# Kernel optimization log

Hardware: AMD Instinct MI355X
Metric: run time of the kernel (lower is better)

## Reference

```python
import jax, jax.numpy as jnp
import numpy as np

# ---- static physical configuration (matches init_kwargs param dict) ----
NX = NY = 513
NL = 3
N_ENS = 4
LX = LY = 5120.0e3
DX = LX / (NX - 1)
DY = LY / (NY - 1)
F0 = 9.375e-5
BETA = 1.754e-11
A2 = 0.0
A4 = 2.0e9
DELTA_EK = 2.0
TAU0 = 2.0e-5
BCCO = 0.2
ZFBC = BCCO / (1.0 + 0.5 * BCCO)
DT = 600.0
NUM_STEPS = 4
HEIGHTS = np.array([350.0, 750.0, 2900.0])
RED_G = np.array([0.025, 0.0125])

JAC_COEF = 1.0 / (F0 * DX * DY)
HYPERDIFF_COEF = A4 / F0**2 / DX**6
BOTTOM_FRICTION_COEF = DELTA_EK / (2.0 * abs(F0) * DX**2 * (-HEIGHTS[-1]))


def _build_constants():
    """Precompute stratification / mode / Helmholtz matrices (float64 numpy, cast to f32)."""
    A = np.zeros((NL, NL))
    A[0, 0] = 1.0 / (HEIGHTS[0] * RED_G[0])
    A[0, 1] = -1.0 / (HEIGHTS[0] * RED_G[0])
    for i in range(1, NL - 1):
        A[i, i - 1] = -1.0 / (HEIGHTS[i] * RED_G[i - 1])
        A[i, i] = 1.0 / HEIGHTS[i] * (1.0 / RED_G[i] + 1.0 / RED_G[i - 1])
        A[i, i + 1] = -1.0 / (HEIGHTS[i] * RED_G[i])
    A[-1, -1] = 1.0 / (HEIGHTS[NL - 1] * RED_G[NL - 2])
    A[-1, -2] = -1.0 / (HEIGHTS[NL - 1] * RED_G[NL - 2])
    lam_r, R = np.linalg.eig(A)
    lam_l, L = np.linalg.eig(A.T)
    lam_r, R, lam_l, L = lam_r.real, R.real, lam_l.real, L.real
    # align left eigenvectors with right eigenvalue ordering (biorthogonality)
    order = np.array([int(np.argmin(np.abs(lam_l - lr))) for lr in lam_r])
    L = L[:, order]
    Cl2m = np.diag(1.0 / np.diag(L.T @ R)) @ L.T
    Cm2l = R
    lambd = lam_r
    # DST-I eigenvalues of the 5-point Laplacian on the interior grid
    xg, yg = np.meshgrid(np.arange(1, NX - 1), np.arange(1, NY - 1), indexing='ij')
    lap_dst = (2 * (np.cos(np.pi / (NX - 1) * xg) - 1) / DX**2
               + 2 * (np.cos(np.pi / (NY - 1) * yg) - 1) / DY**2)
    helm_dst = lap_dst[None] / F0**2 - lambd[:, None, None]  # (nl, nx-2, ny-2)

    def np_dstI1D(x):
        N = x.shape[-1]
        xp = np.zeros(x.shape[:-1] + (N + 2,))
        xp[..., 1:-1] = x
        return np.fft.irfft(-1j * xp, n=2 * (N + 1), axis=-1, norm='ortho')[..., 1:N + 1]

    def np_dstI2D(x):
        return np.swapaxes(np_dstI1D(np.swapaxes(np_dstI1D(x), -1, -2)), -1, -2)

    const = np.ones((NL, NX, NY)) / (NX * NY)
    s = np.zeros_like(const)
    s[:, 1:-1, 1:-1] = np_dstI2D(np_dstI2D(const[:, 1:-1, 1:-1]) / helm_dst)
    hom_sol = (const + s * lambd[:, None, None])[:-1]  # (nl-1, nx, ny)
    M = (Cm2l[1:] - Cm2l[:-1])[:NL - 1, :NL - 1] * hom_sol.mean((1, 2))[None, :]
    alpha = -np.linalg.inv(M) @ (Cm2l[1:, :-1] - Cm2l[:-1, :-1])
    # wind forcing: curl(tau)/(f0*H1) on interior points; tau_y = 0, tau_x(y) only
    tau_x = -TAU0 * np.cos(2 * np.pi * (np.arange(NY) + 0.5) / NY)[None, :] * np.ones((NX, NY))
    dtaux_dy = (tau_x[1:-1, 2:] - tau_x[1:-1, :-2]) / (2 * DY)
    wind = (-dtaux_dy / (F0 * HEIGHTS[0]))[None]  # (1, nx-2, ny-2)
    f32 = lambda a: jnp.asarray(a, jnp.float32)
    return dict(A=f32(A), Cl2m=f32(Cl2m), Cm2l=f32(Cm2l), helmoltz_dst=f32(helm_dst),
                alpha_matrix=f32(alpha), homogeneous_sol=f32(hom_sol), wind_forcing=f32(wind))


# ---------------- stencil ops ----------------

def _pad11(x):
    return jnp.pad(x, [(0, 0)] * (x.ndim - 2) + [(1, 1), (1, 1)])


def laplacian_h_nobc(f):
    # unscaled 5-point Laplacian, interior values only: (..., nx-2, ny-2)
    return (f[..., 2:, 1:-1] + f[..., :-2, 1:-1] + f[..., 1:-1, 2:] + f[..., 1:-1, :-2]
            - 4.0 * f[..., 1:-1, 1:-1])


def laplacian_h(f, fc):
    # full-grid Laplacian with partial-slip boundary treatment (coefficient fc = zfbc)
    lap = _pad11(laplacian_h_nobc(f))
    lap = lap.at[..., 0, :].set(fc * (f[..., 1, :] - f[..., 0, :]))
    lap = lap.at[..., -1, :].set(fc * (f[..., -2, :] - f[..., -1, :]))
    lap = lap.at[..., :, 0].set(fc * (f[..., :, 1] - f[..., :, 0]))
    lap = lap.at[..., :, -1].set(fc * (f[..., :, -2] - f[..., :, -1]))
    return lap


def laplacian_h_boundaries(f, fc):
    # boundary Laplacian values, concat order: x=0 (y interior), x=-1, y=0 (full x), y=-1
    return jnp.concatenate([
        fc * (f[..., 1, 1:-1] - f[..., 0, 1:-1]),
        fc * (f[..., -2, 1:-1] - f[..., -1, 1:-1]),
        fc * (f[..., :, 1] - f[..., :, 0]),
        fc * (f[..., :, -2] - f[..., :, -1])], axis=-1)


def jacobi_h(f, g):
    # Arakawa 9-point Jacobian J(f, g), interior values (..., nx-2, ny-2)
    dx_f = f[..., 2:, :] - f[..., :-2, :]
    dx_g = g[..., 2:, :] - g[..., :-2, :]
    dy_f = f[..., 2:] - f[..., :-2]
    dy_g = g[..., 2:] - g[..., :-2]
    return ((dx_f[..., 1:-1] * dy_g[..., 1:-1, :] - dx_g[..., 1:-1] * dy_f[..., 1:-1, :])
            + (f[..., 2:, 1:-1] * dy_g[..., 2:, :] - f[..., :-2, 1:-1] * dy_g[..., :-2, :])
            - (f[..., 1:-1, 2:] * dx_g[..., 2:] - f[..., 1:-1, :-2] * dx_g[..., :-2])
            + (g[..., 1:-1, 2:] * dx_f[..., 2:] - g[..., 1:-1, :-2] * dx_f[..., :-2])
            - (g[..., 2:, 1:-1] * dy_f[..., 2:, :] - g[..., :-2, 1:-1] * dy_f[..., :-2, :])) / 12.0


# ---------------- DST-I elliptic solve ----------------

def dstI1D(x):
    N = x.shape[-1]
    z = jnp.zeros(x.shape[:-1] + (1,), x.dtype)
    xp = jnp.concatenate([z, x, z], axis=-1)
    return jnp.fft.irfft(-1j * xp.astype(jnp.complex64), n=2 * (N + 1), axis=-1,
                         norm='ortho')[..., 1:N + 1]


def dstI2D(x):
    return jnp.swapaxes(dstI1D(jnp.swapaxes(dstI1D(x), -1, -2)), -1, -2)


def inverse_elliptic_dst(f, op_dst):
    return dstI2D(dstI2D(f) / op_dst)


# ---------------- QG time derivative ----------------

def _time_derivatives(y, A, Cl2m, Cm2l, helm_dst, alpha, hom_sol, wind):
    q, p = y[0], y[1]  # (..., nl, nx, ny)
    # advection + hyperdiffusion RHS on interior (a_2 == 0 branch skipped as in source)
    rhs = JAC_COEF * jacobi_h(q, p)
    delta2_p = laplacian_h(p, ZFBC)
    rhs = rhs - HYPERDIFF_COEF * laplacian_h_nobc(laplacian_h(delta2_p, ZFBC))
    rhs = rhs.at[..., 0:1, :, :].add(wind)
    rhs = rhs.at[..., -1:, :, :].add(BOTTOM_FRICTION_COEF * laplacian_h_nobc(p[..., -1:, :, :]))
    dq = _pad11(rhs)
    # layers -> modes, DST Helmholtz inversion, homogeneous-solution correction
    rhs_h = jnp.einsum('ij,...jxy->...ixy', Cl2m, dq)
    dp_modes = _pad11(inverse_elliptic_dst(rhs_h[..., 1:-1, 1:-1], helm_dst))
    mean_m = dp_modes[..., :-1, :, :].mean((-2, -1))  # (..., nl-1)
    dalpha = jnp.einsum('ij,...j->...i', alpha, mean_m)[..., None, None]
    dp_modes = dp_modes.at[..., :-1, :, :].add(dalpha * hom_sol)
    dp = jnp.einsum('ij,...jxy->...ixy', Cm2l, dp_modes)
    # boundary vorticity update
    dp_bound = jnp.concatenate([dp[..., 0, 1:-1], dp[..., -1, 1:-1],
                                dp[..., :, 0], dp[..., :, -1]], axis=-1)
    delta_p_bound = laplacian_h_boundaries(dp / (F0 * DX)**2, ZFBC)
    dq_bound = delta_p_bound - jnp.einsum('ij,...jl->...il', A, dp_bound)
    ny2 = NY - 2
    dq = dq.at[..., 0, 1:-1].set(dq_bound[..., :ny2])
    dq = dq.at[..., -1, 1:-1].set(dq_bound[..., ny2:2 * ny2])
    dq = dq.at[..., :, 0].set(dq_bound[..., 2 * ny2:2 * ny2 + NX])
    dq = dq.at[..., :, -1].set(dq_bound[..., 2 * ny2 + NX:2 * ny2 + 2 * NX])
    return jnp.stack((dq, dp), 0)


def _forecast(y0, t, A, Cl2m, Cm2l, helm_dst, alpha, hom_sol, wind):
    deriv = lambda y: _time_derivatives(y, A, Cl2m, Cm2l, helm_dst, alpha, hom_sol, wind)

    def step(y, dt_):
        k1 = deriv(y)
        k2 = deriv(y + 0.5 * dt_ * k1)
        k3 = deriv(y + 0.5 * dt_ * k2)
        k4 = deriv(y + dt_ * k3)
        y_next = y + (dt_ / 6.0) * (k1 + 2.0 * k2 + 2.0 * k3 + k4)
        return y_next, y_next

    _, traj = jax.lax.scan(step, y0, t[1:] - t[:-1])
    return jnp.concatenate([y0[None], traj], axis=0)  # (T, 2, n_ens, nl, nx, ny)


def setup_inputs() -> dict:
    key = jax.random.key(0)
    y0 = 0.1 * jax.random.normal(key, (2, N_ENS, NL, NX, NY), dtype=jnp.float32)
    t = jnp.arange(NUM_STEPS + 1, dtype=jnp.float32) * DT
    consts = _build_constants()
    return dict(y0=y0, t=t, **consts)


def reference(y0, t, A, Cl2m, Cm2l, helmoltz_dst, alpha_matrix, homogeneous_sol, wind_forcing):
    return _forecast(y0, t, A, Cl2m, Cm2l, helmoltz_dst, alpha_matrix,
                     homogeneous_sol, wind_forcing)
```

## Files before the change

### kernel.cpp

```cpp
#include <hip/hip_runtime.h>
#include <math.h>

#define NXY 513
#define NIN 511
#define NL3 3
#define NE4 4
#define NB 12
#define GLD 512

static constexpr long FS  = (long)NE4 * NL3 * NXY * NXY;
static constexpr long GSZ = (long)NB * GLD * GLD;
static constexpr int  NSTEPS = 4;

static constexpr double dF0 = 9.375e-05;
static constexpr double dDX = 10000.0;
static constexpr float ZFBCf     = (float)(0.2 / (1.0 + 0.5 * 0.2));
static constexpr float JACCf     = (float)(1.0 / (dF0 * dDX * dDX));
static constexpr float HYPCf     = (float)(2.0e9 / (dF0 * dF0) / (dDX*dDX*dDX*dDX*dDX*dDX));
static constexpr float BFCf      = (float)(2.0 / (2.0 * dF0 * dDX * dDX * (-2900.0)));
static constexpr float INVF0DX2f = (float)(1.0 / ((dF0 * dDX) * (dF0 * dDX)));

typedef short  bf16x8 __attribute__((ext_vector_type(8)));
typedef float  f32x4  __attribute__((ext_vector_type(4)));
typedef unsigned int u32;
typedef __attribute__((address_space(1))) const u32 GAS;
typedef __attribute__((address_space(3))) u32 LAS;
#define GLDS(gp, lp) __builtin_amdgcn_global_load_lds((GAS*)(gp), (LAS*)(lp), 16, 0, 0)

__device__ __forceinline__ unsigned short f2bf(float x) {
    unsigned int u = __float_as_uint(x);
    return (unsigned short)((u + 0x7FFFu + ((u >> 16) & 1u)) >> 16);
}
__device__ __forceinline__ float bf2f(unsigned short h) {
    return __uint_as_float(((unsigned int)h) << 16);
}

__global__ void initS_kernel(unsigned short* __restrict__ Sh, unsigned short* __restrict__ Sl) {
    int k = blockIdx.x * 256 + threadIdx.x;
    int n = blockIdx.y;
    if (k >= GLD || n >= GLD) return;
    float v = 0.f;
    if (n < NIN && k < NIN) {
        int m = ((n + 1) * (k + 1)) & 1023;
        v = (float)(0.0625 * sin(M_PI * (double)m / 512.0));
    }
    unsigned short hs = f2bf(v);
    Sh[n * GLD + k] = hs;
    Sl[n * GLD + k] = f2bf(v - bf2f(hs));
}

__global__ __launch_bounds__(256) void fused_rhs(
    float* __restrict__ kq, const float* __restrict__ q, const float* __restrict__ p,
    const float* __restrict__ wind)
{
    __shared__ float ps[22][72];
    __shared__ float qs[22][72];
    __shared__ float l1[22][72];
    __shared__ float l2[22][72];
    const int c  = blockIdx.z;
    const int x0 = 1 + blockIdx.y * 16;
    const int y0 = 1 + blockIdx.x * 64;
    const int t  = threadIdx.x;
    const size_t off = (size_t)c * NXY * NXY;
    const float* pp = p + off;
    const float* qp = q + off;

    for (int idx = t; idx < 22 * 70; idx += 256) {
        int i = idx / 70, j = idx % 70;
        int gx = x0 - 3 + i, gy = y0 - 3 + j;
        bool in = (gx >= 0 && gx < NXY && gy >= 0 && gy < NXY);
        size_t go = (size_t)gx * NXY + gy;
        ps[i][j] = in ? pp[go] : 0.f;
        qs[i][j] = in ? qp[go] : 0.f;
    }
    __syncthreads();

#define LAPBC(a, i, j, gx, gy) \
    ((gy) == 0       ? ZFBCf * (a[i][(j)+1] - a[i][j]) : \
     (gy) == NXY-1   ? ZFBCf * (a[i][(j)-1] - a[i][j]) : \
     (gx) == 0       ? ZFBCf * (a[(i)+1][j] - a[i][j]) : \
     (gx) == NXY-1   ? ZFBCf * (a[(i)-1][j] - a[i][j]) : \
     a[(i)+1][j] + a[(i)-1][j] + a[i][(j)+1] + a[i][(j)-1] - 4.f * a[i][j])

    for (int idx = t; idx < 20 * 68; idx += 256) {
        int i = 1 + idx / 68, j = 1 + idx % 68;
        int gx = x0 - 3 + i, gy = y0 - 3 + j;
        float v = 0.f;
        if (gx >= 0 && gx < NXY && gy >= 0 && gy < NXY) v = LAPBC(ps, i, j, gx, gy);
        l1[i][j] = v;
    }
    __syncthreads();

    for (int idx = t; idx < 18 * 66; idx += 256) {
        int i = 2 + idx / 66, j = 2 + idx % 66;
        int gx = x0 - 3 + i, gy = y0 - 3 + j;
        float v = 0.f;
        if (gx >= 0 && gx < NXY && gy >= 0 && gy < NXY) v = LAPBC(l1, i, j, gx, gy);
        l2[i][j] = v;
    }
    __syncthreads();
#undef LAPBC

    const int l = c % NL3;
    for (int idx = t; idx < 16 * 64; idx += 256) {
        int i = 3 + idx / 64, j = 3 + idx % 64;
        int gx = x0 - 3 + i, gy = y0 - 3 + j;
        if (gx > NIN || gy > NIN) continue;
        float fmm=qs[i-1][j-1], fm0=qs[i-1][j], fmp=qs[i-1][j+1];
        float f0m=qs[i][j-1],                    f0p=qs[i][j+1];
        float fpm=qs[i+1][j-1], fp0=qs[i+1][j], fpp=qs[i+1][j+1];
        float gmm=ps[i-1][j-1], gm0=ps[i-1][j], gmp=ps[i-1][j+1];
        float g0m=ps[i][j-1],   g00=ps[i][j],   g0p=ps[i][j+1];
        float gpm=ps[i+1][j-1], gp0=ps[i+1][j], gpp=ps[i+1][j+1];
        float J1 = (fp0 - fm0) * (g0p - g0m) - (gp0 - gm0) * (f0p - f0m);
        float J2 = fp0 * (gpp - gpm) - fm0 * (gmp - gmm);
        float J3 = f0p * (gpp - gmp) - f0m * (gpm - gmm);
        float J4 = g0p * (fpp - fmp) - g0m * (fpm - fmm);
        float J5 = gp0 * (fpp - fpm) - gm0 * (fmp - fmm);
        float jac = (J1 + J2 - J3 + J4 - J5) * (1.0f / 12.0f);
        float lap3 = l2[i+1][j] + l2[i-1][j] + l2[i][j+1] + l2[i][j-1] - 4.f * l2[i][j];
        float v = JACCf * jac - HYPCf * lap3;
        if (l == 0)       v += wind[(size_t)(gx-1) * NIN + (gy-1)];
        if (l == NL3-1)   v += BFCf * (gp0 + gm0 + g0p + g0m - 4.f * g00);
        kq[off + (size_t)gx * NXY + gy] = v;
    }
}

__global__ void l2m_kernel(unsigned short* __restrict__ Gh, unsigned short* __restrict__ Gl,
                           const float* __restrict__ kq, const float* __restrict__ Cl2m) {
    int ry = blockIdx.x * blockDim.x + threadIdx.x;
    int rx = blockIdx.y * blockDim.y + threadIdx.y;
    int e = blockIdx.z;
    size_t go = (size_t)(e * NL3) * GLD * GLD + (size_t)rx * GLD + ry;
    if (rx >= NIN || ry >= NIN) {
        for (int i = 0; i < 3; ++i) { Gh[go + (size_t)i*GLD*GLD] = 0; Gl[go + (size_t)i*GLD*GLD] = 0; }
        return;
    }
    size_t base = ((size_t)(e * NL3) * NXY + (rx + 1)) * NXY + (ry + 1);
    float f0 = kq[base];
    float f1 = kq[base + (size_t)NXY*NXY];
    float f2 = kq[base + 2*(size_t)NXY*NXY];
    float v[3];
    v[0] = Cl2m[0]*f0 + Cl2m[1]*f1 + Cl2m[2]*f2;
    v[1] = Cl2m[3]*f0 + Cl2m[4]*f1 + Cl2m[5]*f2;
    v[2] = Cl2m[6]*f0 + Cl2m[7]*f1 + Cl2m[8]*f2;
#pragma unroll
    for (int i = 0; i < 3; ++i) {
        unsigned short hs = f2bf(v[i]);
        Gh[go + (size_t)i*GLD*GLD] = hs;
        Gl[go + (size_t)i*GLD*GLD] = f2bf(v[i] - bf2f(hs));
    }
}

#define EPLD 68
__global__ __launch_bounds__(256, 3) void gemm_dst(
    const unsigned short* __restrict__ Ah, const unsigned short* __restrict__ Al,
    const unsigned short* __restrict__ Sh, const unsigned short* __restrict__ Sl,
    unsigned short* __restrict__ Ch, unsigned short* __restrict__ Cl,
    float* __restrict__ Cf, const float* __restrict__ helm)
{
    __shared__ __attribute__((aligned(16))) char ldsraw[32768];
    float* ep = (float*)ldsraw;
    const int id = blockIdx.x;
    const int nblk = id / 96, rr = id - nblk * 96;
    const int b = rr >> 3, mblk = rr & 7;
    const int m0 = mblk << 6, n0 = nblk << 6;
    const int t = threadIdx.x;
    const int wave = t >> 6, lane = t & 63;
    const int wr = wave >> 1, wc = wave & 1;
    const int lr = lane & 15, g = lane >> 4;
    const unsigned short* Abh = Ah + (size_t)b * 262144;
    const unsigned short* Abl = Al + (size_t)b * 262144;

    const int srow = t >> 2;
    const int scol = ((t & 3) ^ ((srow >> 1) & 3)) * 8;
    const size_t gAe = (size_t)(m0 + srow) * 512 + scol;
    const size_t gBe = (size_t)(n0 + srow) * 512 + scol;
    const int ldbase = wave * 1024;

    auto STAGE = [&](int buf, int kt) {
        char* bb = ldsraw + buf * 16384;
        int ke = kt * 32;
        GLDS(Abh + gAe + ke, bb + ldbase);
        GLDS(Abl + gAe + ke, bb + 4096 + ldbase);
        GLDS(Sh  + gBe + ke, bb + 8192 + ldbase);
        GLDS(Sl  + gBe + ke, bb + 12288 + ldbase);
    };

    f32x4 acc[2][2] = {};
    int abyte[2], bbyte[2];
#pragma unroll
    for (int i = 0; i < 2; ++i) {
        int ar = wr*32 + i*16 + lr;
        abyte[i] = ar*64 + ((g ^ ((ar >> 1) & 3)) * 16);
    }
#pragma unroll
    for (int j = 0; j < 2; ++j) {
        int br = wc*32 + j*16 + lr;
        bbyte[j] = 8192 + br*64 + ((g ^ ((br >> 1) & 3)) * 16);
    }

    STAGE(0, 0);
    __syncthreads();
    for (int it = 0; it < 16; ++it) {
        const int buf = it & 1;
        if (it < 15) STAGE(buf ^ 1, it + 1);
        const char* bb = ldsraw + buf * 16384;
        bf16x8 fbh[2], fbl[2];
#pragma unroll
        for (int j = 0; j < 2; ++j) {
            fbh[j] = *(const bf16x8*)(bb + bbyte[j]);
            fbl[j] = *(const bf16x8*)(bb + 4096 + bbyte[j]);
        }
#pragma unroll
        for (int i = 0; i < 2; ++i) {
            bf16x8 fah = *(const bf16x8*)(bb + abyte[i]);
            bf16x8 fal = *(const bf16x8*)(bb + 4096 + abyte[i]);
#pragma unroll
            for (int j = 0; j < 2; ++j) {
                acc[i][j] = __builtin_amdgcn_mfma_f32_16x16x32_bf16(fah, fbh[j], acc[i][j], 0, 0, 0);
                acc[i][j] = __builtin_amdgcn_mfma_f32_16x16x32_bf16(fah, fbl[j], acc[i][j], 0, 0, 0);
                acc[i][j] = __builtin_amdgcn_mfma_f32_16x16x32_bf16(fal, fbh[j], acc[i][j], 0, 0, 0);
            }
        }
        __syncthreads();
    }

    const int mode = b % NL3;
    const float* hp = helm ? (helm + (size_t)mode * NIN * NIN) : nullptr;
#pragma unroll
    for (int i = 0; i < 2; ++i) {
        int mml = wr*32 + i*16 + 4*g;
#pragma unroll
        for (int j = 0; j < 2; ++j) {
            int nnl = wc*32 + j*16 + lr;
            int nn = n0 + nnl;
            float v[4];
#pragma unroll
            for (int r = 0; r < 4; ++r) v[r] = acc[i][j][r];
            if (hp && nn < NIN) {
                int mmb = m0 + mml;
#pragma unroll
                for (int r = 0; r < 4; ++r)
                    if (mmb + r < NIN) v[r] /= hp[(size_t)nn*NIN + mmb + r];
            }
#pragma unroll
            for (int r = 0; r < 4; ++r) ep[nnl*EPLD + mml + r] = v[r];
        }
    }
    __syncthreads();

#pragma unroll
    for (int c = 0; c < 2; ++c) {
        int chunk = t + 256*c;
        int row = chunk >> 3;
        int cb  = (chunk & 7) * 8;
        float v[8];
#pragma unroll
        for (int k = 0; k < 8; ++k) v[k] = ep[row*EPLD + cb + k];
        size_t co = (size_t)b*262144 + (size_t)(n0 + row)*512 + m0 + cb;
        if (Cf) {
            f32x4 v0 = {v[0], v[1], v[2], v[3]};
            f32x4 v1 = {v[4], v[5], v[6], v[7]};
            *(f32x4*)(Cf + co)     = v0;
            *(f32x4*)(Cf + co + 4) = v1;
        } else {
            unsigned int h[4], lo[4];
#pragma unroll
            for (int k = 0; k < 4; ++k) {
                unsigned short h0 = f2bf(v[2*k]), h1 = f2bf(v[2*k+1]);
                unsigned short l0 = f2bf(v[2*k]-bf2f(h0)), l1 = f2bf(v[2*k+1]-bf2f(h1));
                h[k]  = (unsigned int)h0 | ((unsigned int)h1 << 16);
                lo[k] = (unsigned int)l0 | ((unsigned int)l1 << 16);
            }
            *(uint4*)(Ch + co) = make_uint4(h[0], h[1], h[2], h[3]);
            *(uint4*)(Cl + co) = make_uint4(lo[0], lo[1], lo[2], lo[3]);
        }
    }
}

__global__ void mean_kernel(float* __restrict__ partial, const float* __restrict__ G) {
    int gy = blockIdx.y;
    int e = gy >> 1, m = gy & 1;
    const float* g = G + (size_t)(e * NL3 + m) * GLD * GLD;
    float s = 0.f;
    for (int idx = blockIdx.x * 256 + threadIdx.x; idx < GLD*GLD; idx += 64 * 256)
        s += g[idx];
    __shared__ float red[256];
    red[threadIdx.x] = s; __syncthreads();
    for (int w = 128; w >= 1; w >>= 1) {
        if (threadIdx.x < w) red[threadIdx.x] += red[threadIdx.x + w];
        __syncthreads();
    }
    if (threadIdx.x == 0) partial[gy * 64 + blockIdx.x] = red[0];
}

__global__ void dalpha_kernel(float* __restrict__ dal, const float* __restrict__ partial,
                              const float* __restrict__ alpha) {
    int t = threadIdx.x;
    if (t >= 8) return;
    int e = t >> 1, i = t & 1;
    float s0 = 0.f, s1 = 0.f;
    for (int bk = 0; bk < 64; ++bk) { s0 += partial[(e*2+0)*64 + bk]; s1 += partial[(e*2+1)*64 + bk]; }
    const float inv = 1.0f / ((float)NXY * (float)NXY);
    dal[t] = alpha[i*2+0] * (s0 * inv) + alpha[i*2+1] * (s1 * inv);
}

__global__ void m2l_kernel(float* __restrict__ kp, const float* __restrict__ G,
                           const float* __restrict__ dal, const float* __restrict__ hom,
                           const float* __restrict__ Cm2l) {
    int y = blockIdx.x * blockDim.x + threadIdx.x;
    int x = blockIdx.y * blockDim.y + threadIdx.y;
    int e = blockIdx.z;
    if (x >= NXY || y >= NXY) return;
    float mv[3];
    bool interior = (x >= 1 && x <= NIN && y >= 1 && y <= NIN);
#pragma unroll
    for (int i = 0; i < 3; ++i)
        mv[i] = interior ? G[(size_t)(e*NL3 + i) * GLD * GLD + (size_t)(x-1) * GLD + (y-1)] : 0.f;
    float h0 = hom[(size_t)x * NXY + y];
    float h1 = hom[(size_t)NXY*NXY + (size_t)x * NXY + y];
    mv[0] += dal[e*2 + 0] * h0;
    mv[1] += dal[e*2 + 1] * h1;
#pragma unroll
    for (int l = 0; l < 3; ++l)
        kp[((size_t)(e*NL3 + l) * NXY + x) * NXY + y] =
            Cm2l[l*3+0]*mv[0] + Cm2l[l*3+1]*mv[1] + Cm2l[l*3+2]*mv[2];
}

__global__ void bound_kernel(float* __restrict__ kq, const float* __restrict__ kp,
                             const float* __restrict__ Amat) {
    int pos = blockIdx.x * 256 + threadIdx.x;
    int e = blockIdx.y;
    if (pos >= 2048) return;
    int x, y, xn, yn;
    if (pos < NIN)            { x = 0;      y = pos + 1;        xn = 1;      yn = y; }
    else if (pos < 2*NIN)     { x = NXY-1;  y = pos - NIN + 1;  xn = NXY-2;  yn = y; }
    else if (pos < 2*NIN+NXY) { x = pos - 2*NIN;       y = 0;      xn = x; yn = 1; }
    else                      { x = pos - (2*NIN+NXY); y = NXY-1;  xn = x; yn = NXY-2; }
    float dpb[3], lpb[3];
#pragma unroll
    for (int j = 0; j < 3; ++j) {
        const float* f = kp + (size_t)(e*NL3 + j) * NXY * NXY;
        float c = f[(size_t)x * NXY + y];
        float nb = f[(size_t)xn * NXY + yn];
        dpb[j] = c;
        lpb[j] = ZFBCf * INVF0DX2f * (nb - c);
    }
#pragma unroll
    for (int l = 0; l < 3; ++l) {
        float v = lpb[l] - (Amat[l*3+0]*dpb[0] + Amat[l*3+1]*dpb[1] + Amat[l*3+2]*dpb[2]);
        kq[((size_t)(e*NL3 + l) * NXY + x) * NXY + y] = v;
    }
}

__global__ void rk_fused(float4* __restrict__ o1, float4* __restrict__ o2,
                         const float4* __restrict__ x, const float4* __restrict__ k,
                         float c1, float c2, int accumulate,
                         const float* __restrict__ t, int s, long n4) {
    float dt = t[s+1] - t[s];
    float a1 = c1 * dt, a2 = c2 * dt;
    for (long i = (long)blockIdx.x * blockDim.x + threadIdx.x; i < n4;
         i += (long)gridDim.x * blockDim.x) {
        float4 kk = k[i], xx = x[i];
        float4 b0 = accumulate ? o1[i] : xx;
        o1[i] = make_float4(b0.x + a1*kk.x, b0.y + a1*kk.y, b0.z + a1*kk.z, b0.w + a1*kk.w);
        if (o2) o2[i] = make_float4(xx.x + a2*kk.x, xx.y + a2*kk.y, xx.z + a2*kk.z, xx.w + a2*kk.w);
    }
}

__global__ void copy_kernel(float4* __restrict__ out, const float4* __restrict__ in, long n4) {
    for (long i = (long)blockIdx.x * blockDim.x + threadIdx.x; i < n4;
         i += (long)gridDim.x * blockDim.x)
        out[i] = in[i];
}

extern "C" void kernel_launch(void* const* d_in, const int* in_sizes, int n_in,
                              void* d_out, int out_size, void* d_ws, size_t ws_size,
                              hipStream_t stream) {
    const float* y0    = (const float*)d_in[0];
    const float* tarr  = (const float*)d_in[1];
    const float* Amat  = (const float*)d_in[2];
    const float* Cl2m  = (const float*)d_in[3];
    const float* Cm2l  = (const float*)d_in[4];
    const float* helm  = (const float*)d_in[5];
    const float* alpha = (const float*)d_in[6];
    const float* hom   = (const float*)d_in[7];
    const float* wind  = (const float*)d_in[8];
    float* out = (float*)d_out;
    char* base = (char*)d_ws;

    unsigned short* Sh = (unsigned short*)base;
    unsigned short* Sl = (unsigned short*)(base + 512*1024);
    float* ytmp = (float*)(base + 1024*1024);
    float* kbuf = ytmp + 2*FS;
    char*  REGb = (char*)(kbuf + 2*FS);
    unsigned short* P0h = (unsigned short*)REGb;
    unsigned short* P0l = P0h + GSZ;
    unsigned short* P1h = P0l + GSZ;
    unsigned short* P1l = P1h + GSZ;
    float* R4 = (float*)REGb;
    float* partial = (float*)(REGb + (size_t)2*FS*sizeof(float));
    float* dal = partial + 512;

    const dim3 bSt(64, 4, 1);
    const dim3 gSt4((NXY + 63)/64, (NXY + 3)/4, NE4);
    const dim3 gL2M(8, 128, NE4);
    const dim3 gF(8, 32, NB);
    const dim3 gG(768, 1, 1);
    const long n4 = 2*FS/4;

    initS_kernel<<<dim3(2, GLD), 256, 0, stream>>>(Sh, Sl);
    copy_kernel<<<1024, 256, 0, stream>>>((float4*)out, (const float4*)y0, n4);

    auto deriv = [&](const float* y, float* k) {
        const float* q = y;  const float* p = y + FS;
        float* kq = k;       float* kp = k + FS;
        fused_rhs<<<gF, 256, 0, stream>>>(kq, q, p, wind);
        l2m_kernel<<<gL2M, bSt, 0, stream>>>(P0h, P0l, kq, Cl2m);
        gemm_dst<<<gG, 256, 0, stream>>>(P0h, P0l, Sh, Sl, P1h, P1l, nullptr, nullptr);
        gemm_dst<<<gG, 256, 0, stream>>>(P1h, P1l, Sh, Sl, P0h, P0l, nullptr, helm);
        gemm_dst<<<gG, 256, 0, stream>>>(P0h, P0l, Sh, Sl, P1h, P1l, nullptr, nullptr);
        gemm_dst<<<gG, 256, 0, stream>>>(P1h, P1l, Sh, Sl, nullptr, nullptr, R4, nullptr);
        mean_kernel<<<dim3(64, 8), 256, 0, stream>>>(partial, R4);
        dalpha_kernel<<<1, 64, 0, stream>>>(dal, partial, alpha);
        m2l_kernel<<<gSt4, bSt, 0, stream>>>(kp, R4, dal, hom, Cm2l);
        bound_kernel<<<dim3(8, NE4), 256, 0, stream>>>(kq, kp, Amat);
    };

    for (int s = 0; s < NSTEPS; ++s) {
        float* ycur  = out + (size_t)s * 2 * FS;
        float* ynext = out + (size_t)(s + 1) * 2 * FS;
        deriv(ycur, kbuf);
        rk_fused<<<1024, 256, 0, stream>>>((float4*)ynext, (float4*)ytmp, (const float4*)ycur,
                                           (const float4*)kbuf, 1.f/6.f, 0.5f, 0, tarr, s, n4);
        deriv(ytmp, kbuf);
        rk_fused<<<1024, 256, 0, stream>>>((float4*)ynext, (float4*)ytmp, (const float4*)ycur,
                                           (const float4*)kbuf, 2.f/6.f, 0.5f, 1, tarr, s, n4);
        deriv(ytmp, kbuf);
        rk_fused<<<1024, 256, 0, stream>>>((float4*)ynext, (float4*)ytmp, (const float4*)ycur,
                                           (const float4*)kbuf, 2.f/6.f, 1.0f, 1, tarr, s, n4);
        deriv(ytmp, kbuf);
        rk_fused<<<1024, 256, 0, stream>>>((float4*)ynext, nullptr, (const float4*)ycur,
                                           (const float4*)kbuf, 1.f/6.f, 0.f, 1, tarr, s, n4);
    }
}
```

Measured before the change: 2.264 ms.

## Exploit DST-I even/odd symmetry to halve GEMM work in spectral solve

Uses the symmetry of the DST-I sine matrix (row n and row 510-n differ only by sign on odd/even columns) to split each transform into odd and even half-K GEMMs. Each block computes a half-width output tile and produces both mirrored rows as o+e and o-e. Inputs are stored deinterleaved into even/odd column halves so the K loop runs 8 iterations instead of 16. This roughly halves MFMA work and the reads of the basis matrix. In exchange the index mapping gets more complex, LDS use per block grows, and the last row needs explicit zeroing.

```diff
diff --git a/kernel.cpp b/kernel.cpp
--- a/kernel.cpp
+++ b/kernel.cpp
@@ -35,18 +35,19 @@
     return __uint_as_float(((unsigned int)h) << 16);
 }
 
-__global__ void initS_kernel(unsigned short* __restrict__ Sh, unsigned short* __restrict__ Sl) {
-    int k = blockIdx.x * 256 + threadIdx.x;
-    int n = blockIdx.y;
-    if (k >= GLD || n >= GLD) return;
-    float v = 0.f;
-    if (n < NIN && k < NIN) {
-        int m = ((n + 1) * (k + 1)) & 1023;
-        v = (float)(0.0625 * sin(M_PI * (double)m / 512.0));
-    }
-    unsigned short hs = f2bf(v);
-    Sh[n * GLD + k] = hs;
-    Sl[n * GLD + k] = f2bf(v - bf2f(hs));
+__global__ void initB_kernel(unsigned short* __restrict__ BoH, unsigned short* __restrict__ BoL,
+                             unsigned short* __restrict__ BeH, unsigned short* __restrict__ BeL) {
+    int j = threadIdx.x;
+    int n = blockIdx.x;
+    int idx = n * 256 + j;
+    int mo = ((n + 1) * (2 * j + 1)) & 1023;
+    int me = ((n + 1) * (2 * j + 2)) & 1023;
+    float fo = (float)(0.0625 * sin(M_PI * (double)mo / 512.0));
+    float fe = (float)(0.0625 * sin(M_PI * (double)me / 512.0));
+    unsigned short oh = f2bf(fo);
+    BoH[idx] = oh; BoL[idx] = f2bf(fo - bf2f(oh));
+    unsigned short eh = f2bf(fe);
+    BeH[idx] = eh; BeL[idx] = f2bf(fe - bf2f(eh));
 }
 
 __global__ __launch_bounds__(256) void fused_rhs(
@@ -128,153 +129,188 @@
 
 __global__ void l2m_kernel(unsigned short* __restrict__ Gh, unsigned short* __restrict__ Gl,
                            const float* __restrict__ kq, const float* __restrict__ Cl2m) {
-    int ry = blockIdx.x * blockDim.x + threadIdx.x;
+    int p  = blockIdx.x * blockDim.x + threadIdx.x;
     int rx = blockIdx.y * blockDim.y + threadIdx.y;
     int e = blockIdx.z;
-    size_t go = (size_t)(e * NL3) * GLD * GLD + (size_t)rx * GLD + ry;
-    if (rx >= NIN || ry >= NIN) {
-        for (int i = 0; i < 3; ++i) { Gh[go + (size_t)i*GLD*GLD] = 0; Gl[go + (size_t)i*GLD*GLD] = 0; }
-        return;
-    }
-    size_t base = ((size_t)(e * NL3) * NXY + (rx + 1)) * NXY + (ry + 1);
-    float f0 = kq[base];
-    float f1 = kq[base + (size_t)NXY*NXY];
-    float f2 = kq[base + 2*(size_t)NXY*NXY];
-    float v[3];
-    v[0] = Cl2m[0]*f0 + Cl2m[1]*f1 + Cl2m[2]*f2;
-    v[1] = Cl2m[3]*f0 + Cl2m[4]*f1 + Cl2m[5]*f2;
-    v[2] = Cl2m[6]*f0 + Cl2m[7]*f1 + Cl2m[8]*f2;
+    int ry0 = 2 * p, ry1 = 2 * p + 1;
+    float vA[3] = {0.f, 0.f, 0.f}, vB[3] = {0.f, 0.f, 0.f};
+    if (rx < NIN) {
+        size_t base = ((size_t)(e * NL3) * NXY + (rx + 1)) * NXY;
+        if (ry0 < NIN) {
+            float f0 = kq[base + ry0 + 1];
+            float f1 = kq[base + (size_t)NXY*NXY + ry0 + 1];
+            float f2 = kq[base + 2*(size_t)NXY*NXY + ry0 + 1];
+            vA[0] = Cl2m[0]*f0 + Cl2m[1]*f1 + Cl2m[2]*f2;
+            vA[1] = Cl2m[3]*f0 + Cl2m[4]*f1 + Cl2m[5]*f2;
+            vA[2] = Cl2m[6]*f0 + Cl2m[7]*f1 + Cl2m[8]*f2;
+        }
+        if (ry1 < NIN) {
+            float f0 = kq[base + ry1 + 1];
+            float f1 = kq[base + (size_t)NXY*NXY + ry1 + 1];
+            float f2 = kq[base + 2*(size_t)NXY*NXY + ry1 + 1];
+            vB[0] = Cl2m[0]*f0 + Cl2m[1]*f1 + Cl2m[2]*f2;
+            vB[1] = Cl2m[3]*f0 + Cl2m[4]*f1 + Cl2m[5]*f2;
+            vB[2] = Cl2m[6]*f0 + Cl2m[7]*f1 + Cl2m[8]*f2;
+        }
+    }
 #pragma unroll
     for (int i = 0; i < 3; ++i) {
-        unsigned short hs = f2bf(v[i]);
-        Gh[go + (size_t)i*GLD*GLD] = hs;
-        Gl[go + (size_t)i*GLD*GLD] = f2bf(v[i] - bf2f(hs));
+        size_t pb = (size_t)(e * NL3 + i) * 262144;
+        size_t po = pb + (size_t)rx * 256 + p;
+        size_t pe = po + 131072;
+        unsigned short ha = f2bf(vA[i]);
+        Gh[po] = ha; Gl[po] = f2bf(vA[i] - bf2f(ha));
+        unsigned short hb = f2bf(vB[i]);
+        Gh[pe] = hb; Gl[pe] = f2bf(vB[i] - bf2f(hb));
     }
 }
 
 #define EPLD 68
 __global__ __launch_bounds__(256, 3) void gemm_dst(
     const unsigned short* __restrict__ Ah, const unsigned short* __restrict__ Al,
-    const unsigned short* __restrict__ Sh, const unsigned short* __restrict__ Sl,
+    const unsigned short* __restrict__ BoH, const unsigned short* __restrict__ BoL,
+    const unsigned short* __restrict__ BeH, const unsigned short* __restrict__ BeL,
     unsigned short* __restrict__ Ch, unsigned short* __restrict__ Cl,
     float* __restrict__ Cf, const float* __restrict__ helm)
 {
-    __shared__ __attribute__((aligned(16))) char ldsraw[32768];
-    float* ep = (float*)ldsraw;
+    __shared__ __attribute__((aligned(16))) char lds[49152];
+    float* ep1 = (float*)lds;
+    float* ep2 = ep1 + 32 * EPLD;
     const int id = blockIdx.x;
     const int nblk = id / 96, rr = id - nblk * 96;
     const int b = rr >> 3, mblk = rr & 7;
-    const int m0 = mblk << 6, n0 = nblk << 6;
+    const int m0 = mblk << 6;
+    const int n0t = nblk << 5;
     const int t = threadIdx.x;
-    const int wave = t >> 6, lane = t & 63;
-    const int wr = wave >> 1, wc = wave & 1;
+    const int w = t >> 6, lane = t & 63;
+    const int wn = w >> 1, wm = w & 1;
     const int lr = lane & 15, g = lane >> 4;
-    const unsigned short* Abh = Ah + (size_t)b * 262144;
-    const unsigned short* Abl = Al + (size_t)b * 262144;
-
-    const int srow = t >> 2;
-    const int scol = ((t & 3) ^ ((srow >> 1) & 3)) * 8;
-    const size_t gAe = (size_t)(m0 + srow) * 512 + scol;
-    const size_t gBe = (size_t)(n0 + srow) * 512 + scol;
-    const int ldbase = wave * 1024;
+    const unsigned short* AbH = Ah + (size_t)b * 262144;
+    const unsigned short* AbL = Al + (size_t)b * 262144;
+
+    const int srA = t >> 2;
+    const int scA = ((t & 3) ^ ((srA >> 1) & 3)) * 8;
+    const size_t gA = (size_t)(m0 + srA) * 256 + scA;
+    const int dA = t * 16;
+    const int hid = t & 127;
+    const int srB = hid >> 2;
+    const int scB = ((hid & 3) ^ ((srB >> 1) & 3)) * 8;
+    const size_t gB = (size_t)(n0t + srB) * 256 + scB;
+    const unsigned short* B1 = (t < 128) ? BoH : BoL;
+    const unsigned short* B2 = (t < 128) ? BeH : BeL;
+    const int dB1 = ((t < 128) ? 16384 : 18432) + hid * 16;
+    const int dB2 = ((t < 128) ? 20480 : 22528) + hid * 16;
 
     auto STAGE = [&](int buf, int kt) {
-        char* bb = ldsraw + buf * 16384;
+        char* bb = lds + buf * 24576;
         int ke = kt * 32;
-        GLDS(Abh + gAe + ke, bb + ldbase);
-        GLDS(Abl + gAe + ke, bb + 4096 + ldbase);
-        GLDS(Sh  + gBe + ke, bb + 8192 + ldbase);
-        GLDS(Sl  + gBe + ke, bb + 12288 + ldbase);
+        GLDS(AbH + gA + ke,          bb + dA);
+        GLDS(AbL + gA + ke,          bb + 4096  + dA);
+        GLDS(AbH + 131072 + gA + ke, bb + 8192  + dA);
+        GLDS(AbL + 131072 + gA + ke, bb + 12288 + dA);
+        GLDS(B1 + gB + ke, bb + dB1);
+        GLDS(B2 + gB + ke, bb + dB2);
     };
 
-    f32x4 acc[2][2] = {};
-    int abyte[2], bbyte[2];
+    f32x4 accO[2] = {}, accE[2] = {};
+    int abyte[2];
 #pragma unroll
     for (int i = 0; i < 2; ++i) {
-        int ar = wr*32 + i*16 + lr;
+        int ar = wm*32 + i*16 + lr;
         abyte[i] = ar*64 + ((g ^ ((ar >> 1) & 3)) * 16);
     }
-#pragma unroll
-    for (int j = 0; j < 2; ++j) {
-        int br = wc*32 + j*16 + lr;
-        bbyte[j] = 8192 + br*64 + ((g ^ ((br >> 1) & 3)) * 16);
-    }
+    const int brl = wn*16 + lr;
+    const int bby = brl*64 + ((g ^ ((brl >> 1) & 3)) * 16);
 
     STAGE(0, 0);
     __syncthreads();
-    for (int it = 0; it < 16; ++it) {
+    for (int it = 0; it < 8; ++it) {
         const int buf = it & 1;
-        if (it < 15) STAGE(buf ^ 1, it + 1);
-        const char* bb = ldsraw + buf * 16384;
-        bf16x8 fbh[2], fbl[2];
-#pragma unroll
-        for (int j = 0; j < 2; ++j) {
-            fbh[j] = *(const bf16x8*)(bb + bbyte[j]);
-            fbl[j] = *(const bf16x8*)(bb + 4096 + bbyte[j]);
-        }
+        if (it < 7) STAGE(buf ^ 1, it + 1);
+        const char* bb = lds + buf * 24576;
+        bf16x8 boH = *(const bf16x8*)(bb + 16384 + bby);
+        bf16x8 boL = *(const bf16x8*)(bb + 18432 + bby);
+        bf16x8 beH = *(const bf16x8*)(bb + 20480 + bby);
+        bf16x8 beL = *(const bf16x8*)(bb + 22528 + bby);
 #pragma unroll
         for (int i = 0; i < 2; ++i) {
-            bf16x8 fah = *(const bf16x8*)(bb + abyte[i]);
-            bf16x8 fal = *(const bf16x8*)(bb + 4096 + abyte[i]);
-#pragma unroll
-            for (int j = 0; j < 2; ++j) {
-                acc[i][j] = __builtin_amdgcn_mfma_f32_16x16x32_bf16(fah, fbh[j], acc[i][j], 0, 0, 0);
-                acc[i][j] = __builtin_amdgcn_mfma_f32_16x16x32_bf16(fah, fbl[j], acc[i][j], 0, 0, 0);
-                acc[i][j] = __builtin_amdgcn_mfma_f32_16x16x32_bf16(fal, fbh[j], acc[i][j], 0, 0, 0);
-            }
+            bf16x8 aoH = *(const bf16x8*)(bb + abyte[i]);
+            bf16x8 aoL = *(const bf16x8*)(bb + 4096  + abyte[i]);
+            bf16x8 aeH = *(const bf16x8*)(bb + 8192  + abyte[i]);
+            bf16x8 aeL = *(const bf16x8*)(bb + 12288 + abyte[i]);
+            accO[i] = __builtin_amdgcn_mfma_f32_16x16x32_bf16(aoH, boH, accO[i], 0, 0, 0);
+            accO[i] = __builtin_amdgcn_mfma_f32_16x16x32_bf16(aoH, boL, accO[i], 0, 0, 0);
+            accO[i] = __builtin_amdgcn_mfma_f32_16x16x32_bf16(aoL, boH, accO[i], 0, 0, 0);
+            accE[i] = __builtin_amdgcn_mfma_f32_16x16x32_bf16(aeH, beH, accE[i], 0, 0, 0);
+            accE[i] = __builtin_amdgcn_mfma_f32_16x16x32_bf16(aeH, beL, accE[i], 0, 0, 0);
+            accE[i] = __builtin_amdgcn_mfma_f32_16x16x32_bf16(aeL, beH, accE[i], 0, 0, 0);
         }
         __syncthreads();
     }
 
     const int mode = b % NL3;
     const float* hp = helm ? (helm + (size_t)mode * NIN * NIN) : nullptr;
+    const int nl = wn*16 + lr;
+    const int r1g = n0t + nl;
+    const int r2g = 510 - n0t - nl;
 #pragma unroll
     for (int i = 0; i < 2; ++i) {
-        int mml = wr*32 + i*16 + 4*g;
-#pragma unroll
-        for (int j = 0; j < 2; ++j) {
-            int nnl = wc*32 + j*16 + lr;
-            int nn = n0 + nnl;
-            float v[4];
-#pragma unroll
-            for (int r = 0; r < 4; ++r) v[r] = acc[i][j][r];
-            if (hp && nn < NIN) {
-                int mmb = m0 + mml;
-#pragma unroll
-                for (int r = 0; r < 4; ++r)
-                    if (mmb + r < NIN) v[r] /= hp[(size_t)nn*NIN + mmb + r];
+        int ml = wm*32 + i*16 + 4*g;
+#pragma unroll
+        for (int r = 0; r < 4; ++r) {
+            float o = accO[i][r], e = accE[i][r];
+            float v1 = o + e, v2 = o - e;
+            int mg = m0 + ml + r;
+            if (hp && mg < NIN) {
+                v1 /= hp[(size_t)r1g * NIN + mg];
+                v2 /= hp[(size_t)r2g * NIN + mg];
             }
-#pragma unroll
-            for (int r = 0; r < 4; ++r) ep[nnl*EPLD + mml + r] = v[r];
+            ep1[nl*EPLD + ml + r] = v1;
+            ep2[nl*EPLD + ml + r] = v2;
         }
     }
     __syncthreads();
 
-#pragma unroll
-    for (int c = 0; c < 2; ++c) {
-        int chunk = t + 256*c;
-        int row = chunk >> 3;
-        int cb  = (chunk & 7) * 8;
-        float v[8];
-#pragma unroll
-        for (int k = 0; k < 8; ++k) v[k] = ep[row*EPLD + cb + k];
-        size_t co = (size_t)b*262144 + (size_t)(n0 + row)*512 + m0 + cb;
+    {
+        const int row = t >> 3;
+        const int cb = (t & 7) * 8;
+        const int r1 = n0t + row;
+        const int r2 = 510 - n0t - row;
+        float v1[8], v2[8];
+#pragma unroll
+        for (int k = 0; k < 8; ++k) { v1[k] = ep1[row*EPLD + cb + k]; v2[k] = ep2[row*EPLD + cb + k]; }
         if (Cf) {
-            f32x4 v0 = {v[0], v[1], v[2], v[3]};
-            f32x4 v1 = {v[4], v[5], v[6], v[7]};
-            *(f32x4*)(Cf + co)     = v0;
-            *(f32x4*)(Cf + co + 4) = v1;
+            size_t c1 = (size_t)b*262144 + (size_t)r1*512 + m0 + cb;
+            size_t c2 = (size_t)b*262144 + (size_t)r2*512 + m0 + cb;
+            f32x4 a0 = {v1[0], v1[1], v1[2], v1[3]};
+            f32x4 a1 = {v1[4], v1[5], v1[6], v1[7]};
+            f32x4 b0 = {v2[0], v2[1], v2[2], v2[3]};
+            f32x4 b1 = {v2[4], v2[5], v2[6], v2[7]};
+            *(f32x4*)(Cf + c1) = a0; *(f32x4*)(Cf + c1 + 4) = a1;
+            *(f32x4*)(Cf + c2) = b0; *(f32x4*)(Cf + c2 + 4) = b1;
+            if (nblk == 0 && t < 64) Cf[(size_t)b*262144 + (size_t)511*512 + m0 + t] = 0.f;
         } else {
-            unsigned int h[4], lo[4];
-#pragma unroll
-            for (int k = 0; k < 4; ++k) {
-                unsigned short h0 = f2bf(v[2*k]), h1 = f2bf(v[2*k+1]);
-                unsigned short l0 = f2bf(v[2*k]-bf2f(h0)), l1 = f2bf(v[2*k+1]-bf2f(h1));
-                h[k]  = (unsigned int)h0 | ((unsigned int)h1 << 16);
-                lo[k] = (unsigned int)l0 | ((unsigned int)l1 << 16);
+            auto STROW = [&](int rrow, const float* v) {
+                size_t po = (size_t)b*262144 + (size_t)rrow*256 + ((m0 + cb) >> 1);
+                size_t pe = po + 131072;
+                unsigned short eh[4], el[4], oh[4], ol[4];
+#pragma unroll
+                for (int k = 0; k < 4; ++k) {
+                    float ve = v[2*k], vo = v[2*k+1];
+                    eh[k] = f2bf(ve); el[k] = f2bf(ve - bf2f(eh[k]));
+                    oh[k] = f2bf(vo); ol[k] = f2bf(vo - bf2f(oh[k]));
+                }
+                *(uint2*)(Ch + po) = make_uint2((u32)eh[0] | ((u32)eh[1] << 16), (u32)eh[2] | ((u32)eh[3] << 16));
+                *(uint2*)(Cl + po) = make_uint2((u32)el[0] | ((u32)el[1] << 16), (u32)el[2] | ((u32)el[3] << 16));
+                *(uint2*)(Ch + pe) = make_uint2((u32)oh[0] | ((u32)oh[1] << 16), (u32)oh[2] | ((u32)oh[3] << 16));
+                *(uint2*)(Cl + pe) = make_uint2((u32)ol[0] | ((u32)ol[1] << 16), (u32)ol[2] | ((u32)ol[3] << 16));
+            };
+            STROW(r1, v1);
+            STROW(r2, v2);
+            if (nblk == 0 && t < 32) {
+                size_t z = (size_t)b*262144 + (size_t)511*256 + (m0 >> 1) + t;
+                Ch[z] = 0; Cl[z] = 0; Ch[z + 131072] = 0; Cl[z + 131072] = 0;
             }
-            *(uint4*)(Ch + co) = make_uint4(h[0], h[1], h[2], h[3]);
-            *(uint4*)(Cl + co) = make_uint4(lo[0], lo[1], lo[2], lo[3]);
         }
     }
 }
@@ -390,8 +426,10 @@
     float* out = (float*)d_out;
     char* base = (char*)d_ws;
 
-    unsigned short* Sh = (unsigned short*)base;
-    unsigned short* Sl = (unsigned short*)(base + 512*1024);
+    unsigned short* BoH = (unsigned short*)base;
+    unsigned short* BoL = BoH + 65536;
+    unsigned short* BeH = BoL + 65536;
+    unsigned short* BeL = BeH + 65536;
     float* ytmp = (float*)(base + 1024*1024);
     float* kbuf = ytmp + 2*FS;
     char*  REGb = (char*)(kbuf + 2*FS);
@@ -405,12 +443,12 @@
 
     const dim3 bSt(64, 4, 1);
     const dim3 gSt4((NXY + 63)/64, (NXY + 3)/4, NE4);
-    const dim3 gL2M(8, 128, NE4);
+    const dim3 gL2M(4, 128, NE4);
     const dim3 gF(8, 32, NB);
     const dim3 gG(768, 1, 1);
     const long n4 = 2*FS/4;
 
-    initS_kernel<<<dim3(2, GLD), 256, 0, stream>>>(Sh, Sl);
+    initB_kernel<<<256, 256, 0, stream>>>(BoH, BoL, BeH, BeL);
     copy_kernel<<<1024, 256, 0, stream>>>((float4*)out, (const float4*)y0, n4);
 
     auto deriv = [&](const float* y, float* k) {
@@ -418,10 +456,10 @@
         float* kq = k;       float* kp = k + FS;
         fused_rhs<<<gF, 256, 0, stream>>>(kq, q, p, wind);
         l2m_kernel<<<gL2M, bSt, 0, stream>>>(P0h, P0l, kq, Cl2m);
-        gemm_dst<<<gG, 256, 0, stream>>>(P0h, P0l, Sh, Sl, P1h, P1l, nullptr, nullptr);
-        gemm_dst<<<gG, 256, 0, stream>>>(P1h, P1l, Sh, Sl, P0h, P0l, nullptr, helm);
-        gemm_dst<<<gG, 256, 0, stream>>>(P0h, P0l, Sh, Sl, P1h, P1l, nullptr, nullptr);
-        gemm_dst<<<gG, 256, 0, stream>>>(P1h, P1l, Sh, Sl, nullptr, nullptr, R4, nullptr);
+        gemm_dst<<<gG, 256, 0, stream>>>(P0h, P0l, BoH, BoL, BeH, BeL, P1h, P1l, nullptr, nullptr);
+        gemm_dst<<<gG, 256, 0, stream>>>(P1h, P1l, BoH, BoL, BeH, BeL, P0h, P0l, nullptr, helm);
+        gemm_dst<<<gG, 256, 0, stream>>>(P0h, P0l, BoH, BoL, BeH, BeL, P1h, P1l, nullptr, nullptr);
+        gemm_dst<<<gG, 256, 0, stream>>>(P1h, P1l, BoH, BoL, BeH, BeL, nullptr, nullptr, R4, nullptr);
         mean_kernel<<<dim3(64, 8), 256, 0, stream>>>(partial, R4);
         dalpha_kernel<<<1, 64, 0, stream>>>(dal, partial, alpha);
         m2l_kernel<<<gSt4, bSt, 0, stream>>>(kp, R4, dal, hom, Cm2l);
```

New measurement: 2.147 ms. 1.05x faster.
